# Optimization experiments

Hardware: AMD Instinct MI355X
Metric: run time of the kernel (lower is better)

The kernel has to match this reference:

```python
import jax, jax.numpy as jnp
import numpy as np

N_NODES = 50000
N_EDGES = 1600000
N_GRAPHS = 512
HID = 64


def _mlp_params(key, din, dout, scale=0.1):
    k1, k2, k3 = jax.random.split(key, 3)
    return (
        jax.random.normal(k1, (din, HID), jnp.float32) * scale, jnp.zeros((HID,), jnp.float32),
        jax.random.normal(k2, (HID, HID), jnp.float32) * scale, jnp.zeros((HID,), jnp.float32),
        jax.random.normal(k3, (HID, dout), jnp.float32) * scale, jnp.zeros((dout,), jnp.float32),
    )


def _mlp(x, w1, b1, w2, b2, w3, b3, out_act=None):
    h = jax.nn.relu(x @ w1 + b1)
    h = jax.nn.relu(h @ w2 + b2)
    o = h @ w3 + b3
    return o if out_act is None else out_act(o)


def setup_inputs() -> dict:
    key = jax.random.key(0)
    ks = jax.random.split(key, 8)
    nf = jax.random.normal(ks[0], (N_NODES, 1), jnp.float32)
    ef = jax.random.normal(ks[1], (N_EDGES, 1), jnp.float32)
    src = jax.random.randint(ks[2], (N_EDGES,), 0, N_NODES)
    dst = jax.random.randint(ks[3], (N_EDGES,), 0, N_NODES)
    graph_id = jnp.sort(jax.random.randint(ks[4], (N_NODES,), 0, N_GRAPHS))
    e_w1, e_b1, e_w2, e_b2, e_w3, e_b3 = _mlp_params(ks[5], 3, 1)   # edge model: [src_nf, dst_nf, ef] -> msg
    n_w1, n_b1, n_w2, n_b2, n_w3, n_b3 = _mlp_params(ks[6], 2, 1)   # node model: [nf, agg] -> unf
    m_w1, m_b1, m_w2, m_b2, m_w3, m_b3 = _mlp_params(ks[7], 1, 1)   # node-wise MLP with Sigmoid out_act
    return dict(nf=nf, ef=ef, src=src, dst=dst, graph_id=graph_id,
                e_w1=e_w1, e_b1=e_b1, e_w2=e_w2, e_b2=e_b2, e_w3=e_w3, e_b3=e_b3,
                n_w1=n_w1, n_b1=n_b1, n_w2=n_w2, n_b2=n_b2, n_w3=n_w3, n_b3=n_b3,
                m_w1=m_w1, m_b1=m_b1, m_w2=m_w2, m_b2=m_b2, m_w3=m_w3, m_b3=m_b3)


def reference(nf, ef, src, dst, graph_id,
              e_w1, e_b1, e_w2, e_b2, e_w3, e_b3,
              n_w1, n_b1, n_w2, n_b2, n_w3, n_b3,
              m_w1, m_b1, m_w2, m_b2, m_w3, m_b3):
    # MPNN layer: message on edges, sum-aggregate to dst nodes, node update
    em_in = jnp.concatenate([nf[src], nf[dst], ef], axis=-1)          # [E, 3]
    msg = _mlp(em_in, e_w1, e_b1, e_w2, e_b2, e_w3, e_b3)             # [E, 1]
    agg = jax.ops.segment_sum(msg, dst, num_segments=N_NODES)        # [N, 1]
    unf = _mlp(jnp.concatenate([nf, agg], axis=-1),
               n_w1, n_b1, n_w2, n_b2, n_w3, n_b3)                    # [N, 1]
    # node-wise MLP with Sigmoid output activation
    node_out = _mlp(unf, m_w1, m_b1, m_w2, m_b2, m_w3, m_b3,
                    out_act=jax.nn.sigmoid)                           # [N, 1]
    # sum readout per graph, then final sigmoid
    rd = jax.ops.segment_sum(node_out, graph_id, num_segments=N_GRAPHS)  # [G, 1]
    return jax.nn.sigmoid(rd)
```

## Files before the change

kernel.cpp:

```cpp
#include <hip/hip_runtime.h>
#include <math.h>

#define HID 64
#define BKT_SHIFT 13
#define BKT_RANGE 8192
#define CCHUNK 32

typedef __attribute__((ext_vector_type(8))) short short8;
typedef __attribute__((ext_vector_type(4))) float f32x4;
typedef unsigned long long ull;

union FragU {
    uint4 q;
    short8 v;
    uint32_t u[4];
};

__device__ __forceinline__ uint32_t cvt_pk_bf16(float lo, float hi) {
    uint32_t r;
    asm("v_cvt_pk_bf16_f32 %0, %1, %2" : "=v"(r) : "v"(lo), "v"(hi));
    return r;
}
__device__ __forceinline__ float bf16lo_f(uint32_t u) { return __uint_as_float(u << 16); }
__device__ __forceinline__ float bf16hi_f(uint32_t u) { return __uint_as_float(u & 0xFFFF0000u); }
__device__ __forceinline__ unsigned short bf16_of(float v) {
    return (unsigned short)(cvt_pk_bf16(v, 0.f) & 0xFFFFu);
}

__global__ void prep_kernel(
    const float* __restrict__ w1,  const float* __restrict__ b1,  const float* __restrict__ w2,
    const float* __restrict__ nw1, const float* __restrict__ nb1, const float* __restrict__ nw2,
    const float* __restrict__ mw1, const float* __restrict__ mb1, const float* __restrict__ mw2,
    unsigned short* __restrict__ w1x,  unsigned short* __restrict__ w2T,
    unsigned short* __restrict__ nw1x, unsigned short* __restrict__ nw2T,
    unsigned short* __restrict__ mw1x, unsigned short* __restrict__ mw2T)
{
    int t = blockIdx.x * 256 + threadIdx.x;
    if (t < 4096) {
        int j = t >> 6, k = t & 63;
        w2T [t] = bf16_of(w2 [k * HID + j]);
        nw2T[t] = bf16_of(nw2[k * HID + j]);
        mw2T[t] = bf16_of(mw2[k * HID + j]);
    }
    if (t < 512) {
        int j = t >> 3, k = t & 7;
        float ve = k == 0 ? w1[j] : k == 1 ? w1[HID + j] : k == 2 ? w1[2 * HID + j] : k == 3 ? b1[j] : 0.f;
        float vn = k == 0 ? nw1[j] : k == 1 ? nw1[HID + j] : k == 2 ? nb1[j] : 0.f;
        float vm = k == 0 ? mw1[j] : k == 1 ? mb1[j] : 0.f;
        w1x [t] = bf16_of(ve);
        nw1x[t] = bf16_of(vn);
        mw1x[t] = bf16_of(vm);
    }
}

__global__ __launch_bounds__(256, 4) void edge_mfma2_kernel(
    const float* __restrict__ nf, const float* __restrict__ ef,
    const int* __restrict__ src, const int* __restrict__ dst,
    const unsigned short* __restrict__ w1x, const unsigned short* __restrict__ w2T,
    const float* __restrict__ b2, const float* __restrict__ w3, const float* __restrict__ b3,
    uint2* __restrict__ recs, ull* __restrict__ offs,
    float* __restrict__ aggFb, int E, int B, int mode)
{
    __shared__ uint2 tile[4][16][16];

    const int tid  = threadIdx.x;
    const int lane = tid & 63;
    const int wid  = tid >> 6;
    const int g    = lane >> 4;
    const int eL   = lane & 15;

    FragU af1[4];
#pragma unroll
    for (int t = 0; t < 4; ++t) {
        uint4 q = *(const uint4*)&w1x[(t * 16 + eL) * 8];
        af1[t].q = (g == 0) ? q : make_uint4(0, 0, 0, 0);
    }
    FragU af2[4][2];
#pragma unroll
    for (int t = 0; t < 4; ++t)
#pragma unroll
        for (int h = 0; h < 2; ++h)
            af2[t][h].q = *(const uint4*)&w2T[(t * 16 + eL) * 64 + h * 32 + g * 8];

    f32x4 b2v4[4];
    uint32_t w3p[8];
#pragma unroll
    for (int t = 0; t < 4; ++t) {
        int j = t * 16 + g * 4;
        b2v4[t] = *(const f32x4*)&b2[j];
        f32x4 wv = *(const f32x4*)&w3[j];
        w3p[2 * t]     = cvt_pk_bf16(wv[0], wv[1]);
        w3p[2 * t + 1] = cvt_pk_bf16(wv[2], wv[3]);
    }
    const float b3c = b3[0];

    const int e0   = blockIdx.x * 256;
    const int eidx = e0 + tid;
    const int ei   = eidx < E ? eidx : E - 1;
    const int dmine = dst[ei];
    const float a = nf[src[ei]];
    const float b = nf[dmine];
    const float c = ef[ei];

    float mymsg = 0.f;

#pragma unroll
    for (int s = 0; s < 4; ++s) {
        float av = __shfl(a, s * 16 + eL);
        float bv = __shfl(b, s * 16 + eL);
        float cv = __shfl(c, s * 16 + eL);
        FragU bin;
        bin.u[0] = (g == 0) ? cvt_pk_bf16(av, bv) : 0u;
        bin.u[1] = (g == 0) ? cvt_pk_bf16(cv, 1.0f) : 0u;
        bin.u[2] = 0u; bin.u[3] = 0u;

#pragma unroll
        for (int t = 0; t < 4; ++t) {
            f32x4 h4 = __builtin_amdgcn_mfma_f32_16x16x32_bf16(
                af1[t].v, bin.v, (f32x4){0.f, 0.f, 0.f, 0.f}, 0, 0, 0);
            uint32_t p0 = cvt_pk_bf16(fmaxf(h4[0], 0.f), fmaxf(h4[1], 0.f));
            uint32_t p1 = cvt_pk_bf16(fmaxf(h4[2], 0.f), fmaxf(h4[3], 0.f));
            tile[wid][eL][(4 * t + g) ^ ((eL & 7) << 1)] = make_uint2(p0, p1);
        }

        FragU bf0, bf1;
        {
            const uint4* row = (const uint4*)&tile[wid][eL][0];
            bf0.q = row[(g)     ^ (eL & 7)];
            bf1.q = row[(4 + g) ^ (eL & 7)];
        }

        float p = 0.f;
#pragma unroll
        for (int t = 0; t < 4; ++t) {
            f32x4 ac = __builtin_amdgcn_mfma_f32_16x16x32_bf16(af2[t][0].v, bf0.v, b2v4[t], 0, 0, 0);
            ac = __builtin_amdgcn_mfma_f32_16x16x32_bf16(af2[t][1].v, bf1.v, ac, 0, 0, 0);
            p = fmaf(fmaxf(ac[0], 0.f), bf16lo_f(w3p[2 * t]),     p);
            p = fmaf(fmaxf(ac[1], 0.f), bf16hi_f(w3p[2 * t]),     p);
            p = fmaf(fmaxf(ac[2], 0.f), bf16lo_f(w3p[2 * t + 1]), p);
            p = fmaf(fmaxf(ac[3], 0.f), bf16hi_f(w3p[2 * t + 1]), p);
        }
        p += __shfl_xor(p, 16);
        p += __shfl_xor(p, 32);
        if (s == g) mymsg = p + b3c;
    }

    const bool valid = eidx < E;

    if (mode == 1) {
        if (valid) atomicAdd(&aggFb[dmine], mymsg);
        return;
    }

    const int bkt = dmine >> BKT_SHIFT;
    const ull lt = (1ull << lane) - 1;
    int myslot = 0;
    int off = 0;
    uint32_t pack_lo = 0, pack_hi = 0;
    for (int b = 0; b < B; ++b) {
        if (b < 4) pack_lo |= (uint32_t)off << (8 * b);
        else       pack_hi |= (uint32_t)off << (8 * (b - 4));
        ull m = __ballot(valid && bkt == b);
        if (valid && bkt == b) myslot = off + (int)__popcll(m & lt);
        off += (int)__popcll(m);
    }
    pack_hi |= (uint32_t)off << 24;

    const size_t wgl = (size_t)blockIdx.x * 4 + wid;
    if (valid) recs[wgl * 64 + myslot] = make_uint2((uint32_t)dmine, __float_as_uint(mymsg));
    if (lane == 0) offs[wgl] = ((ull)pack_hi << 32) | (ull)pack_lo;
}

__global__ __launch_bounds__(256) void bucket_accum_kernel(
    const uint2* __restrict__ recs, const ull* __restrict__ offs,
    float* __restrict__ partial, int NW, int B)
{
    __shared__ float acc[BKT_RANGE];

    const int b = blockIdx.x / CCHUNK;
    const int c = blockIdx.x % CCHUNK;

    for (int i = threadIdx.x; i < BKT_RANGE; i += 256) acc[i] = 0.f;
    __syncthreads();

    const int wpc = (NW + CCHUNK - 1) / CCHUNK;
    const int w0 = c * wpc;
    const int w1 = (w0 + wpc < NW) ? w0 + wpc : NW;
    const int nb = b + 1;
    const int base_node = b << BKT_SHIFT;

    for (int w = w0 + threadIdx.x; w < w1; w += 256) {
        ull ov = offs[w];
        uint32_t lo = (uint32_t)ov, hi = (uint32_t)(ov >> 32);
        int ob = (int)(((b  < 4) ? (lo >> (8 * b))  : (hi >> (8 * (b  - 4)))) & 0xFF);
        int oe = (int)(((nb < 4) ? (lo >> (8 * nb)) : (hi >> (8 * (nb - 4)))) & 0xFF);
        const uint2* rb = recs + (size_t)w * 64;
        for (int r = ob; r < oe; ++r) {
            uint2 rec = rb[r];
            atomicAdd(&acc[(int)rec.x - base_node], __uint_as_float(rec.y));
        }
    }
    __syncthreads();

    float* pb = partial + ((size_t)b * CCHUNK + c) * BKT_RANGE;
    for (int i = threadIdx.x; i < BKT_RANGE; i += 256) pb[i] = acc[i];
}

__global__ __launch_bounds__(256) void bucket_reduce_kernel(
    const float* __restrict__ partial, float* __restrict__ agg, int N)
{
    int n = blockIdx.x * 256 + threadIdx.x;
    if (n >= N) return;
    int b = n >> BKT_SHIFT, nl = n & (BKT_RANGE - 1);
    const float* p = partial + (size_t)b * CCHUNK * BKT_RANGE + nl;
    float s = 0.f;
#pragma unroll 8
    for (int c = 0; c < CCHUNK; ++c) s += p[(size_t)c * BKT_RANGE];
    agg[n] = s;
}

__global__ __launch_bounds__(64, 2) void node_mfma2_kernel(
    const float* __restrict__ nf, const float* __restrict__ agg,
    const int* __restrict__ gid,
    const unsigned short* __restrict__ nw1x, const unsigned short* __restrict__ nw2T,
    const float* __restrict__ nb2, const float* __restrict__ nw3, const float* __restrict__ nb3,
    const unsigned short* __restrict__ mw1x, const unsigned short* __restrict__ mw2T,
    const float* __restrict__ mb2, const float* __restrict__ mw3, const float* __restrict__ mb3,
    float* __restrict__ rd, int N)
{
    __shared__ uint2 tile[16][16];

    const int lane = threadIdx.x;
    const int g    = lane >> 4;
    const int eL   = lane & 15;

    const int n0 = blockIdx.x * 16;
    const int nn = n0 + eL < N ? n0 + eL : N - 1;
    const float x0 = nf[nn];
    const float x1 = agg[nn];

    float unf, o;

    {
        FragU af1[4], af2[4][2];
        f32x4 b2v4[4]; uint32_t w3p[8];
#pragma unroll
        for (int t = 0; t < 4; ++t) {
            uint4 q = *(const uint4*)&nw1x[(t * 16 + eL) * 8];
            af1[t].q = (g == 0) ? q : make_uint4(0, 0, 0, 0);
#pragma unroll
            for (int h = 0; h < 2; ++h)
                af2[t][h].q = *(const uint4*)&nw2T[(t * 16 + eL) * 64 + h * 32 + g * 8];
            int j = t * 16 + g * 4;
            b2v4[t] = *(const f32x4*)&nb2[j];
            f32x4 wv = *(const f32x4*)&nw3[j];
            w3p[2 * t]     = cvt_pk_bf16(wv[0], wv[1]);
            w3p[2 * t + 1] = cvt_pk_bf16(wv[2], wv[3]);
        }
        FragU bin;
        bin.u[0] = (g == 0) ? cvt_pk_bf16(x0, x1) : 0u;
        bin.u[1] = (g == 0) ? cvt_pk_bf16(1.0f, 0.f) : 0u;
        bin.u[2] = 0u; bin.u[3] = 0u;

#pragma unroll
        for (int t = 0; t < 4; ++t) {
            f32x4 h4 = __builtin_amdgcn_mfma_f32_16x16x32_bf16(
                af1[t].v, bin.v, (f32x4){0.f, 0.f, 0.f, 0.f}, 0, 0, 0);
            uint32_t p0 = cvt_pk_bf16(fmaxf(h4[0], 0.f), fmaxf(h4[1], 0.f));
            uint32_t p1 = cvt_pk_bf16(fmaxf(h4[2], 0.f), fmaxf(h4[3], 0.f));
            tile[eL][(4 * t + g) ^ ((eL & 7) << 1)] = make_uint2(p0, p1);
        }
        FragU bf0, bf1;
        {
            const uint4* row = (const uint4*)&tile[eL][0];
            bf0.q = row[(g)     ^ (eL & 7)];
            bf1.q = row[(4 + g) ^ (eL & 7)];
        }
        float p = 0.f;
#pragma unroll
        for (int t = 0; t < 4; ++t) {
            f32x4 ac = __builtin_amdgcn_mfma_f32_16x16x32_bf16(af2[t][0].v, bf0.v, b2v4[t], 0, 0, 0);
            ac = __builtin_amdgcn_mfma_f32_16x16x32_bf16(af2[t][1].v, bf1.v, ac, 0, 0, 0);
            p = fmaf(fmaxf(ac[0], 0.f), bf16lo_f(w3p[2 * t]),     p);
            p = fmaf(fmaxf(ac[1], 0.f), bf16hi_f(w3p[2 * t]),     p);
            p = fmaf(fmaxf(ac[2], 0.f), bf16lo_f(w3p[2 * t + 1]), p);
            p = fmaf(fmaxf(ac[3], 0.f), bf16hi_f(w3p[2 * t + 1]), p);
        }
        p += __shfl_xor(p, 16);
        p += __shfl_xor(p, 32);
        unf = p + nb3[0];
    }

    {
        FragU af1[4], af2[4][2];
        f32x4 b2v4[4]; uint32_t w3p[8];
#pragma unroll
        for (int t = 0; t < 4; ++t) {
            uint4 q = *(const uint4*)&mw1x[(t * 16 + eL) * 8];
            af1[t].q = (g == 0) ? q : make_uint4(0, 0, 0, 0);
#pragma unroll
            for (int h = 0; h < 2; ++h)
                af2[t][h].q = *(const uint4*)&mw2T[(t * 16 + eL) * 64 + h * 32 + g * 8];
            int j = t * 16 + g * 4;
            b2v4[t] = *(const f32x4*)&mb2[j];
            f32x4 wv = *(const f32x4*)&mw3[j];
            w3p[2 * t]     = cvt_pk_bf16(wv[0], wv[1]);
            w3p[2 * t + 1] = cvt_pk_bf16(wv[2], wv[3]);
        }
        FragU bin;
        bin.u[0] = (g == 0) ? cvt_pk_bf16(unf, 1.0f) : 0u;
        bin.u[1] = 0u; bin.u[2] = 0u; bin.u[3] = 0u;

#pragma unroll
        for (int t = 0; t < 4; ++t) {
            f32x4 h4 = __builtin_amdgcn_mfma_f32_16x16x32_bf16(
                af1[t].v, bin.v, (f32x4){0.f, 0.f, 0.f, 0.f}, 0, 0, 0);
            uint32_t p0 = cvt_pk_bf16(fmaxf(h4[0], 0.f), fmaxf(h4[1], 0.f));
            uint32_t p1 = cvt_pk_bf16(fmaxf(h4[2], 0.f), fmaxf(h4[3], 0.f));
            tile[eL][(4 * t + g) ^ ((eL & 7) << 1)] = make_uint2(p0, p1);
        }
        FragU bf0, bf1;
        {
            const uint4* row = (const uint4*)&tile[eL][0];
            bf0.q = row[(g)     ^ (eL & 7)];
            bf1.q = row[(4 + g) ^ (eL & 7)];
        }
        float p = 0.f;
#pragma unroll
        for (int t = 0; t < 4; ++t) {
            f32x4 ac = __builtin_amdgcn_mfma_f32_16x16x32_bf16(af2[t][0].v, bf0.v, b2v4[t], 0, 0, 0);
            ac = __builtin_amdgcn_mfma_f32_16x16x32_bf16(af2[t][1].v, bf1.v, ac, 0, 0, 0);
            p = fmaf(fmaxf(ac[0], 0.f), bf16lo_f(w3p[2 * t]),     p);
            p = fmaf(fmaxf(ac[1], 0.f), bf16hi_f(w3p[2 * t]),     p);
            p = fmaf(fmaxf(ac[2], 0.f), bf16lo_f(w3p[2 * t + 1]), p);
            p = fmaf(fmaxf(ac[3], 0.f), bf16hi_f(w3p[2 * t + 1]), p);
        }
        p += __shfl_xor(p, 16);
        p += __shfl_xor(p, 32);
        o = p + mb3[0];
    }

    float node_out = 1.0f / (1.0f + expf(-o));

    {
        int gg = gid[nn];
        float v = (n0 + eL < N && g == 0) ? node_out : 0.f;
#pragma unroll
        for (int d = 1; d < 16; d <<= 1) {
            float vup = __shfl_up(v, d);
            int   gup = __shfl_up(gg, d);
            if (lane >= d && lane < 16 && gup == gg) v += vup;
        }
        if (lane < 16 && n0 + lane < N) {
            int gdn = __shfl_down(gg, 1);
            bool tail = (lane == 15) || (n0 + lane + 1 >= N) || (gdn != gg);
            if (tail) atomicAdd(&rd[gg], v);
        }
    }
}

__global__ void readout_kernel(const float* __restrict__ rd,
                               float* __restrict__ out, int G)
{
    int g = blockIdx.x * blockDim.x + threadIdx.x;
    if (g < G) out[g] = 1.0f / (1.0f + expf(-rd[g]));
}

extern "C" void kernel_launch(void* const* d_in, const int* in_sizes, int n_in,
                              void* d_out, int out_size, void* d_ws, size_t ws_size,
                              hipStream_t stream)
{
    const float* nf  = (const float*)d_in[0];
    const float* ef  = (const float*)d_in[1];
    const int*   src = (const int*)  d_in[2];
    const int*   dst = (const int*)  d_in[3];
    const int*   gid = (const int*)  d_in[4];

    const float* e_w1 = (const float*)d_in[5];
    const float* e_b1 = (const float*)d_in[6];
    const float* e_w2 = (const float*)d_in[7];
    const float* e_b2 = (const float*)d_in[8];
    const float* e_w3 = (const float*)d_in[9];
    const float* e_b3 = (const float*)d_in[10];

    const float* n_w1 = (const float*)d_in[11];
    const float* n_b1 = (const float*)d_in[12];
    const float* n_w2 = (const float*)d_in[13];
    const float* n_b2 = (const float*)d_in[14];
    const float* n_w3 = (const float*)d_in[15];
    const float* n_b3 = (const float*)d_in[16];

    const float* m_w1 = (const float*)d_in[17];
    const float* m_b1 = (const float*)d_in[18];
    const float* m_w2 = (const float*)d_in[19];
    const float* m_b2 = (const float*)d_in[20];
    const float* m_w3 = (const float*)d_in[21];
    const float* m_b3 = (const float*)d_in[22];

    const int N = in_sizes[0];
    const int E = in_sizes[2];
    const int G = out_size;

    const int NW = (E + 63) / 64;
    const int B  = (N + BKT_RANGE - 1) / BKT_RANGE;

    size_t wts_b  = 32 * 1024;
    size_t recs_b = (size_t)NW * 64 * sizeof(uint2);
    size_t offs_b = (size_t)NW * sizeof(ull);
    size_t part_b = (size_t)B * CCHUNK * BKT_RANGE * sizeof(float);
    size_t need   = wts_b + recs_b + offs_b + part_b + ((size_t)N + G) * sizeof(float);
    bool bucketok = (B <= 8) && (need <= ws_size);

    char* wp = (char*)d_ws;
    unsigned short* w1x  = (unsigned short*)(wp);
    unsigned short* nw1x = (unsigned short*)(wp + 1024);
    unsigned short* mw1x = (unsigned short*)(wp + 2048);
    unsigned short* w2T  = (unsigned short*)(wp + 4096);
    unsigned short* nw2T = (unsigned short*)(wp + 4096 + 8192);
    unsigned short* mw2T = (unsigned short*)(wp + 4096 + 16384);

    float* out = (float*)d_out;

    prep_kernel<<<16, 256, 0, stream>>>(
        e_w1, e_b1, e_w2, n_w1, n_b1, n_w2, m_w1, m_b1, m_w2,
        w1x, w2T, nw1x, nw2T, mw1x, mw2T);

    if (bucketok) {
        uint2* recs    = (uint2*)(wp + wts_b);
        ull*   offs    = (ull*)(wp + wts_b + recs_b);
        float* partial = (float*)(wp + wts_b + recs_b + offs_b);
        float* agg     = (float*)(wp + wts_b + recs_b + offs_b + part_b);
        float* rd      = agg + N;

        hipMemsetAsync(rd, 0, (size_t)G * sizeof(float), stream);

        edge_mfma2_kernel<<<(E + 255) / 256, 256, 0, stream>>>(
            nf, ef, src, dst, w1x, w2T, e_b2, e_w3, e_b3,
            recs, offs, nullptr, E, B, 0);

        bucket_accum_kernel<<<B * CCHUNK, 256, 0, stream>>>(
            recs, offs, partial, NW, B);

        bucket_reduce_kernel<<<(N + 255) / 256, 256, 0, stream>>>(
            partial, agg, N);

        node_mfma2_kernel<<<(N + 15) / 16, 64, 0, stream>>>(
            nf, agg, gid,
            nw1x, nw2T, n_b2, n_w3, n_b3,
            mw1x, mw2T, m_b2, m_w3, m_b3,
            rd, N);

        readout_kernel<<<(G + 255) / 256, 256, 0, stream>>>(rd, out, G);
    } else {
        float* agg = (float*)(wp + wts_b);
        float* rd  = agg + N;

        hipMemsetAsync(agg, 0, ((size_t)N + G) * sizeof(float), stream);

        edge_mfma2_kernel<<<(E + 255) / 256, 256, 0, stream>>>(
            nf, ef, src, dst, w1x, w2T, e_b2, e_w3, e_b3,
            nullptr, nullptr, agg, E, B, 1);

        node_mfma2_kernel<<<(N + 15) / 16, 64, 0, stream>>>(
            nf, agg, gid,
            nw1x, nw2T, n_b2, n_w3, n_b3,
            mw1x, mw2T, m_b2, m_w3, m_b3,
            rd, N);

        readout_kernel<<<(G + 255) / 256, 256, 0, stream>>>(rd, out, G);
    }
}
```

Measured before the change: 87.40 us.

## Persistent edge kernel with gather prefetch; widen node kernel to four waves

The edge kernel becomes a grid-stride persistent kernel capped at 1024 blocks. It prefetches the next batch's src/dst/ef and the nf gathers while computing the MLP on the current batch, and splits the layer-1 and layer-2 phases across four LDS tiles so the gathers can overlap the compute. The node kernel moves from 16 nodes per 64-thread block to 256 nodes per 256-thread block, with a 64-lane segmented scan for the readout, which cuts block count and atomics. In exchange, LDS use grows and the occupancy hint for the edge kernel drops from 4 to 2, which raises register pressure.

```diff
diff --git a/kernel.cpp b/kernel.cpp
--- a/kernel.cpp
+++ b/kernel.cpp
@@ -53,15 +53,15 @@
     }
 }
 
-__global__ __launch_bounds__(256, 4) void edge_mfma2_kernel(
+__global__ __launch_bounds__(256, 2) void edge_mfma3_kernel(
     const float* __restrict__ nf, const float* __restrict__ ef,
     const int* __restrict__ src, const int* __restrict__ dst,
     const unsigned short* __restrict__ w1x, const unsigned short* __restrict__ w2T,
     const float* __restrict__ b2, const float* __restrict__ w3, const float* __restrict__ b3,
     uint2* __restrict__ recs, ull* __restrict__ offs,
-    float* __restrict__ aggFb, int E, int B, int mode)
-{
-    __shared__ uint2 tile[4][16][16];
+    float* __restrict__ aggFb, int E, int B, int nbatch, int mode)
+{
+    __shared__ uint2 tile[4][4][16][16];
 
     const int tid  = threadIdx.x;
     const int lane = tid & 63;
@@ -94,81 +94,97 @@
     }
     const float b3c = b3[0];
 
-    const int e0   = blockIdx.x * 256;
-    const int eidx = e0 + tid;
-    const int ei   = eidx < E ? eidx : E - 1;
-    const int dmine = dst[ei];
-    const float a = nf[src[ei]];
-    const float b = nf[dmine];
-    const float c = ef[ei];
-
-    float mymsg = 0.f;
-
-#pragma unroll
-    for (int s = 0; s < 4; ++s) {
-        float av = __shfl(a, s * 16 + eL);
-        float bv = __shfl(b, s * 16 + eL);
-        float cv = __shfl(c, s * 16 + eL);
-        FragU bin;
-        bin.u[0] = (g == 0) ? cvt_pk_bf16(av, bv) : 0u;
-        bin.u[1] = (g == 0) ? cvt_pk_bf16(cv, 1.0f) : 0u;
-        bin.u[2] = 0u; bin.u[3] = 0u;
-
-#pragma unroll
-        for (int t = 0; t < 4; ++t) {
-            f32x4 h4 = __builtin_amdgcn_mfma_f32_16x16x32_bf16(
-                af1[t].v, bin.v, (f32x4){0.f, 0.f, 0.f, 0.f}, 0, 0, 0);
-            uint32_t p0 = cvt_pk_bf16(fmaxf(h4[0], 0.f), fmaxf(h4[1], 0.f));
-            uint32_t p1 = cvt_pk_bf16(fmaxf(h4[2], 0.f), fmaxf(h4[3], 0.f));
-            tile[wid][eL][(4 * t + g) ^ ((eL & 7) << 1)] = make_uint2(p0, p1);
-        }
-
-        FragU bf0, bf1;
-        {
-            const uint4* row = (const uint4*)&tile[wid][eL][0];
+    int bi   = blockIdx.x;
+    if (bi >= nbatch) return;
+    int eidx = bi * 256 + tid;
+    int ei   = eidx < E ? eidx : E - 1;
+    int dcur = dst[ei];
+    float a  = nf[src[ei]];
+    float b  = nf[dcur];
+    float c  = ef[ei];
+
+    for (;;) {
+        const int nbi   = bi + gridDim.x;
+        const bool hn   = nbi < nbatch;
+        const int neidx = hn ? nbi * 256 + tid : eidx;
+        const int nei   = neidx < E ? neidx : E - 1;
+        const int ns    = src[nei];
+        const int nd    = dst[nei];
+        const float ncf = ef[nei];
+
+#pragma unroll
+        for (int s = 0; s < 4; ++s) {
+            float av = __shfl(a, s * 16 + eL);
+            float bv = __shfl(b, s * 16 + eL);
+            float cv = __shfl(c, s * 16 + eL);
+            FragU bin;
+            bin.u[0] = (g == 0) ? cvt_pk_bf16(av, bv) : 0u;
+            bin.u[1] = (g == 0) ? cvt_pk_bf16(cv, 1.0f) : 0u;
+            bin.u[2] = 0u; bin.u[3] = 0u;
+#pragma unroll
+            for (int t = 0; t < 4; ++t) {
+                f32x4 h4 = __builtin_amdgcn_mfma_f32_16x16x32_bf16(
+                    af1[t].v, bin.v, (f32x4){0.f, 0.f, 0.f, 0.f}, 0, 0, 0);
+                uint32_t p0 = cvt_pk_bf16(fmaxf(h4[0], 0.f), fmaxf(h4[1], 0.f));
+                uint32_t p1 = cvt_pk_bf16(fmaxf(h4[2], 0.f), fmaxf(h4[3], 0.f));
+                tile[wid][s][eL][(4 * t + g) ^ ((eL & 7) << 1)] = make_uint2(p0, p1);
+            }
+        }
+
+        const float na = nf[ns];
+        const float nb = nf[nd];
+
+        float mymsg = 0.f;
+#pragma unroll
+        for (int s = 0; s < 4; ++s) {
+            const uint4* row = (const uint4*)&tile[wid][s][eL][0];
+            FragU bf0, bf1;
             bf0.q = row[(g)     ^ (eL & 7)];
             bf1.q = row[(4 + g) ^ (eL & 7)];
-        }
-
-        float p = 0.f;
-#pragma unroll
-        for (int t = 0; t < 4; ++t) {
-            f32x4 ac = __builtin_amdgcn_mfma_f32_16x16x32_bf16(af2[t][0].v, bf0.v, b2v4[t], 0, 0, 0);
-            ac = __builtin_amdgcn_mfma_f32_16x16x32_bf16(af2[t][1].v, bf1.v, ac, 0, 0, 0);
-            p = fmaf(fmaxf(ac[0], 0.f), bf16lo_f(w3p[2 * t]),     p);
-            p = fmaf(fmaxf(ac[1], 0.f), bf16hi_f(w3p[2 * t]),     p);
-            p = fmaf(fmaxf(ac[2], 0.f), bf16lo_f(w3p[2 * t + 1]), p);
-            p = fmaf(fmaxf(ac[3], 0.f), bf16hi_f(w3p[2 * t + 1]), p);
-        }
-        p += __shfl_xor(p, 16);
-        p += __shfl_xor(p, 32);
-        if (s == g) mymsg = p + b3c;
-    }
-
-    const bool valid = eidx < E;
-
-    if (mode == 1) {
-        if (valid) atomicAdd(&aggFb[dmine], mymsg);
-        return;
-    }
-
-    const int bkt = dmine >> BKT_SHIFT;
-    const ull lt = (1ull << lane) - 1;
-    int myslot = 0;
-    int off = 0;
-    uint32_t pack_lo = 0, pack_hi = 0;
-    for (int b = 0; b < B; ++b) {
-        if (b < 4) pack_lo |= (uint32_t)off << (8 * b);
-        else       pack_hi |= (uint32_t)off << (8 * (b - 4));
-        ull m = __ballot(valid && bkt == b);
-        if (valid && bkt == b) myslot = off + (int)__popcll(m & lt);
-        off += (int)__popcll(m);
-    }
-    pack_hi |= (uint32_t)off << 24;
-
-    const size_t wgl = (size_t)blockIdx.x * 4 + wid;
-    if (valid) recs[wgl * 64 + myslot] = make_uint2((uint32_t)dmine, __float_as_uint(mymsg));
-    if (lane == 0) offs[wgl] = ((ull)pack_hi << 32) | (ull)pack_lo;
+
+            float p = 0.f;
+#pragma unroll
+            for (int t = 0; t < 4; ++t) {
+                f32x4 ac = __builtin_amdgcn_mfma_f32_16x16x32_bf16(af2[t][0].v, bf0.v, b2v4[t], 0, 0, 0);
+                ac = __builtin_amdgcn_mfma_f32_16x16x32_bf16(af2[t][1].v, bf1.v, ac, 0, 0, 0);
+                p = fmaf(fmaxf(ac[0], 0.f), bf16lo_f(w3p[2 * t]),     p);
+                p = fmaf(fmaxf(ac[1], 0.f), bf16hi_f(w3p[2 * t]),     p);
+                p = fmaf(fmaxf(ac[2], 0.f), bf16lo_f(w3p[2 * t + 1]), p);
+                p = fmaf(fmaxf(ac[3], 0.f), bf16hi_f(w3p[2 * t + 1]), p);
+            }
+            p += __shfl_xor(p, 16);
+            p += __shfl_xor(p, 32);
+            if (s == g) mymsg = p + b3c;
+        }
+
+        const bool valid = eidx < E;
+
+        if (mode == 1) {
+            if (valid) atomicAdd(&aggFb[dcur], mymsg);
+        } else {
+            const int bkt = dcur >> BKT_SHIFT;
+            const ull lt = (1ull << lane) - 1;
+            int myslot = 0;
+            int off = 0;
+            uint32_t pack_lo = 0, pack_hi = 0;
+            for (int bb = 0; bb < B; ++bb) {
+                if (bb < 4) pack_lo |= (uint32_t)off << (8 * bb);
+                else        pack_hi |= (uint32_t)off << (8 * (bb - 4));
+                ull m = __ballot(valid && bkt == bb);
+                if (valid && bkt == bb) myslot = off + (int)__popcll(m & lt);
+                off += (int)__popcll(m);
+            }
+            pack_hi |= (uint32_t)off << 24;
+
+            const size_t wgl = (size_t)bi * 4 + wid;
+            if (valid) recs[wgl * 64 + myslot] = make_uint2((uint32_t)dcur, __float_as_uint(mymsg));
+            if (lane == 0) offs[wgl] = ((ull)pack_hi << 32) | (ull)pack_lo;
+        }
+
+        if (!hn) break;
+        bi = nbi; eidx = neidx; ei = nei;
+        a = na; b = nb; c = ncf; dcur = nd;
+    }
 }
 
 __global__ __launch_bounds__(256) void bucket_accum_kernel(
@@ -219,7 +235,7 @@
     agg[n] = s;
 }
 
-__global__ __launch_bounds__(64, 2) void node_mfma2_kernel(
+__global__ __launch_bounds__(256, 2) void node_mfma3_kernel(
     const float* __restrict__ nf, const float* __restrict__ agg,
     const int* __restrict__ gid,
     const unsigned short* __restrict__ nw1x, const unsigned short* __restrict__ nw2T,
@@ -228,18 +244,21 @@
     const float* __restrict__ mb2, const float* __restrict__ mw3, const float* __restrict__ mb3,
     float* __restrict__ rd, int N)
 {
-    __shared__ uint2 tile[16][16];
-
-    const int lane = threadIdx.x;
+    __shared__ uint2 tile[4][4][16][16];
+
+    const int tid  = threadIdx.x;
+    const int lane = tid & 63;
+    const int wid  = tid >> 6;
     const int g    = lane >> 4;
     const int eL   = lane & 15;
 
-    const int n0 = blockIdx.x * 16;
-    const int nn = n0 + eL < N ? n0 + eL : N - 1;
-    const float x0 = nf[nn];
-    const float x1 = agg[nn];
-
-    float unf, o;
+    const int idx = blockIdx.x * 256 + tid;
+    const int i   = idx < N ? idx : N - 1;
+    const float x0 = nf[i];
+    const float x1 = agg[i];
+    const int   gg = gid[i];
+
+    float myunf = 0.f, o = 0.f;
 
     {
         FragU af1[4], af2[4][2];
@@ -257,38 +276,44 @@
             w3p[2 * t]     = cvt_pk_bf16(wv[0], wv[1]);
             w3p[2 * t + 1] = cvt_pk_bf16(wv[2], wv[3]);
         }
-        FragU bin;
-        bin.u[0] = (g == 0) ? cvt_pk_bf16(x0, x1) : 0u;
-        bin.u[1] = (g == 0) ? cvt_pk_bf16(1.0f, 0.f) : 0u;
-        bin.u[2] = 0u; bin.u[3] = 0u;
-
-#pragma unroll
-        for (int t = 0; t < 4; ++t) {
-            f32x4 h4 = __builtin_amdgcn_mfma_f32_16x16x32_bf16(
-                af1[t].v, bin.v, (f32x4){0.f, 0.f, 0.f, 0.f}, 0, 0, 0);
-            uint32_t p0 = cvt_pk_bf16(fmaxf(h4[0], 0.f), fmaxf(h4[1], 0.f));
-            uint32_t p1 = cvt_pk_bf16(fmaxf(h4[2], 0.f), fmaxf(h4[3], 0.f));
-            tile[eL][(4 * t + g) ^ ((eL & 7) << 1)] = make_uint2(p0, p1);
-        }
-        FragU bf0, bf1;
-        {
-            const uint4* row = (const uint4*)&tile[eL][0];
+
+#pragma unroll
+        for (int s = 0; s < 4; ++s) {
+            float av = __shfl(x0, s * 16 + eL);
+            float bv = __shfl(x1, s * 16 + eL);
+            FragU bin;
+            bin.u[0] = (g == 0) ? cvt_pk_bf16(av, bv) : 0u;
+            bin.u[1] = (g == 0) ? cvt_pk_bf16(1.0f, 0.f) : 0u;
+            bin.u[2] = 0u; bin.u[3] = 0u;
+#pragma unroll
+            for (int t = 0; t < 4; ++t) {
+                f32x4 h4 = __builtin_amdgcn_mfma_f32_16x16x32_bf16(
+                    af1[t].v, bin.v, (f32x4){0.f, 0.f, 0.f, 0.f}, 0, 0, 0);
+                uint32_t p0 = cvt_pk_bf16(fmaxf(h4[0], 0.f), fmaxf(h4[1], 0.f));
+                uint32_t p1 = cvt_pk_bf16(fmaxf(h4[2], 0.f), fmaxf(h4[3], 0.f));
+                tile[wid][s][eL][(4 * t + g) ^ ((eL & 7) << 1)] = make_uint2(p0, p1);
+            }
+        }
+#pragma unroll
+        for (int s = 0; s < 4; ++s) {
+            const uint4* row = (const uint4*)&tile[wid][s][eL][0];
+            FragU bf0, bf1;
             bf0.q = row[(g)     ^ (eL & 7)];
             bf1.q = row[(4 + g) ^ (eL & 7)];
-        }
-        float p = 0.f;
-#pragma unroll
-        for (int t = 0; t < 4; ++t) {
-            f32x4 ac = __builtin_amdgcn_mfma_f32_16x16x32_bf16(af2[t][0].v, bf0.v, b2v4[t], 0, 0, 0);
-            ac = __builtin_amdgcn_mfma_f32_16x16x32_bf16(af2[t][1].v, bf1.v, ac, 0, 0, 0);
-            p = fmaf(fmaxf(ac[0], 0.f), bf16lo_f(w3p[2 * t]),     p);
-            p = fmaf(fmaxf(ac[1], 0.f), bf16hi_f(w3p[2 * t]),     p);
-            p = fmaf(fmaxf(ac[2], 0.f), bf16lo_f(w3p[2 * t + 1]), p);
-            p = fmaf(fmaxf(ac[3], 0.f), bf16hi_f(w3p[2 * t + 1]), p);
-        }
-        p += __shfl_xor(p, 16);
-        p += __shfl_xor(p, 32);
-        unf = p + nb3[0];
+            float p = 0.f;
+#pragma unroll
+            for (int t = 0; t < 4; ++t) {
+                f32x4 ac = __builtin_amdgcn_mfma_f32_16x16x32_bf16(af2[t][0].v, bf0.v, b2v4[t], 0, 0, 0);
+                ac = __builtin_amdgcn_mfma_f32_16x16x32_bf16(af2[t][1].v, bf1.v, ac, 0, 0, 0);
+                p = fmaf(fmaxf(ac[0], 0.f), bf16lo_f(w3p[2 * t]),     p);
+                p = fmaf(fmaxf(ac[1], 0.f), bf16hi_f(w3p[2 * t]),     p);
+                p = fmaf(fmaxf(ac[2], 0.f), bf16lo_f(w3p[2 * t + 1]), p);
+                p = fmaf(fmaxf(ac[3], 0.f), bf16hi_f(w3p[2 * t + 1]), p);
+            }
+            p += __shfl_xor(p, 16);
+            p += __shfl_xor(p, 32);
+            if (s == g) myunf = p + nb3[0];
+        }
     }
 
     {
@@ -307,55 +332,60 @@
             w3p[2 * t]     = cvt_pk_bf16(wv[0], wv[1]);
             w3p[2 * t + 1] = cvt_pk_bf16(wv[2], wv[3]);
         }
-        FragU bin;
-        bin.u[0] = (g == 0) ? cvt_pk_bf16(unf, 1.0f) : 0u;
-        bin.u[1] = 0u; bin.u[2] = 0u; bin.u[3] = 0u;
-
-#pragma unroll
-        for (int t = 0; t < 4; ++t) {
-            f32x4 h4 = __builtin_amdgcn_mfma_f32_16x16x32_bf16(
-                af1[t].v, bin.v, (f32x4){0.f, 0.f, 0.f, 0.f}, 0, 0, 0);
-            uint32_t p0 = cvt_pk_bf16(fmaxf(h4[0], 0.f), fmaxf(h4[1], 0.f));
-            uint32_t p1 = cvt_pk_bf16(fmaxf(h4[2], 0.f), fmaxf(h4[3], 0.f));
-            tile[eL][(4 * t + g) ^ ((eL & 7) << 1)] = make_uint2(p0, p1);
-        }
-        FragU bf0, bf1;
-        {
-            const uint4* row = (const uint4*)&tile[eL][0];
+
+#pragma unroll
+        for (int s = 0; s < 4; ++s) {
+            float uv = __shfl(myunf, s * 16 + eL);
+            FragU bin;
+            bin.u[0] = (g == 0) ? cvt_pk_bf16(uv, 1.0f) : 0u;
+            bin.u[1] = 0u; bin.u[2] = 0u; bin.u[3] = 0u;
+#pragma unroll
+            for (int t = 0; t < 4; ++t) {
+                f32x4 h4 = __builtin_amdgcn_mfma_f32_16x16x32_bf16(
+                    af1[t].v, bin.v, (f32x4){0.f, 0.f, 0.f, 0.f}, 0, 0, 0);
+                uint32_t p0 = cvt_pk_bf16(fmaxf(h4[0], 0.f), fmaxf(h4[1], 0.f));
+                uint32_t p1 = cvt_pk_bf16(fmaxf(h4[2], 0.f), fmaxf(h4[3], 0.f));
+                tile[wid][s][eL][(4 * t + g) ^ ((eL & 7) << 1)] = make_uint2(p0, p1);
+            }
+        }
+#pragma unroll
+        for (int s = 0; s < 4; ++s) {
+            const uint4* row = (const uint4*)&tile[wid][s][eL][0];
+            FragU bf0, bf1;
             bf0.q = row[(g)     ^ (eL & 7)];
             bf1.q = row[(4 + g) ^ (eL & 7)];
-        }
-        float p = 0.f;
-#pragma unroll
-        for (int t = 0; t < 4; ++t) {
-            f32x4 ac = __builtin_amdgcn_mfma_f32_16x16x32_bf16(af2[t][0].v, bf0.v, b2v4[t], 0, 0, 0);
-            ac = __builtin_amdgcn_mfma_f32_16x16x32_bf16(af2[t][1].v, bf1.v, ac, 0, 0, 0);
-            p = fmaf(fmaxf(ac[0], 0.f), bf16lo_f(w3p[2 * t]),     p);
-            p = fmaf(fmaxf(ac[1], 0.f), bf16hi_f(w3p[2 * t]),     p);
-            p = fmaf(fmaxf(ac[2], 0.f), bf16lo_f(w3p[2 * t + 1]), p);
-            p = fmaf(fmaxf(ac[3], 0.f), bf16hi_f(w3p[2 * t + 1]), p);
-        }
-        p += __shfl_xor(p, 16);
-        p += __shfl_xor(p, 32);
-        o = p + mb3[0];
-    }
-
-    float node_out = 1.0f / (1.0f + expf(-o));
+            float p = 0.f;
+#pragma unroll
+            for (int t = 0; t < 4; ++t) {
+                f32x4 ac = __builtin_amdgcn_mfma_f32_16x16x32_bf16(af2[t][0].v, bf0.v, b2v4[t], 0, 0, 0);
+                ac = __builtin_amdgcn_mfma_f32_16x16x32_bf16(af2[t][1].v, bf1.v, ac, 0, 0, 0);
+                p = fmaf(fmaxf(ac[0], 0.f), bf16lo_f(w3p[2 * t]),     p);
+                p = fmaf(fmaxf(ac[1], 0.f), bf16hi_f(w3p[2 * t]),     p);
+                p = fmaf(fmaxf(ac[2], 0.f), bf16lo_f(w3p[2 * t + 1]), p);
+                p = fmaf(fmaxf(ac[3], 0.f), bf16hi_f(w3p[2 * t + 1]), p);
+            }
+            p += __shfl_xor(p, 16);
+            p += __shfl_xor(p, 32);
+            if (s == g) o = p + mb3[0];
+        }
+    }
+
+    const float node_out = 1.0f / (1.0f + expf(-o));
 
     {
-        int gg = gid[nn];
-        float v = (n0 + eL < N && g == 0) ? node_out : 0.f;
-#pragma unroll
-        for (int d = 1; d < 16; d <<= 1) {
+        const bool ok = idx < N;
+        float v = ok ? node_out : 0.0f;
+        int ggv = gg;
+#pragma unroll
+        for (int d = 1; d < 64; d <<= 1) {
             float vup = __shfl_up(v, d);
-            int   gup = __shfl_up(gg, d);
-            if (lane >= d && lane < 16 && gup == gg) v += vup;
-        }
-        if (lane < 16 && n0 + lane < N) {
-            int gdn = __shfl_down(gg, 1);
-            bool tail = (lane == 15) || (n0 + lane + 1 >= N) || (gdn != gg);
-            if (tail) atomicAdd(&rd[gg], v);
-        }
+            int   gup = __shfl_up(ggv, d);
+            if (lane >= d && gup == ggv) v += vup;
+        }
+        int gdn = __shfl_down(ggv, 1);
+        bool tail = (lane == 63) || (gdn != ggv);
+        if (tail)
+            atomicAdd(&rd[ggv], v);
     }
 }
 
@@ -401,6 +431,7 @@
     const int E = in_sizes[2];
     const int G = out_size;
 
+    const int nbatch = (E + 255) / 256;
     const int NW = (E + 63) / 64;
     const int B  = (N + BKT_RANGE - 1) / BKT_RANGE;
 
@@ -425,6 +456,8 @@
         e_w1, e_b1, e_w2, n_w1, n_b1, n_w2, m_w1, m_b1, m_w2,
         w1x, w2T, nw1x, nw2T, mw1x, mw2T);
 
+    int egrid = nbatch < 1024 ? nbatch : 1024;
+
     if (bucketok) {
         uint2* recs    = (uint2*)(wp + wts_b);
         ull*   offs    = (ull*)(wp + wts_b + recs_b);
@@ -434,9 +467,9 @@
 
         hipMemsetAsync(rd, 0, (size_t)G * sizeof(float), stream);
 
-        edge_mfma2_kernel<<<(E + 255) / 256, 256, 0, stream>>>(
+        edge_mfma3_kernel<<<egrid, 256, 0, stream>>>(
             nf, ef, src, dst, w1x, w2T, e_b2, e_w3, e_b3,
-            recs, offs, nullptr, E, B, 0);
+            recs, offs, nullptr, E, B, nbatch, 0);
 
         bucket_accum_kernel<<<B * CCHUNK, 256, 0, stream>>>(
             recs, offs, partial, NW, B);
@@ -444,7 +477,7 @@
         bucket_reduce_kernel<<<(N + 255) / 256, 256, 0, stream>>>(
             partial, agg, N);
 
-        node_mfma2_kernel<<<(N + 15) / 16, 64, 0, stream>>>(
+        node_mfma3_kernel<<<(N + 255) / 256, 256, 0, stream>>>(
             nf, agg, gid,
             nw1x, nw2T, n_b2, n_w3, n_b3,
             mw1x, mw2T, m_b2, m_w3, m_b3,
@@ -457,11 +490,11 @@
 
         hipMemsetAsync(agg, 0, ((size_t)N + G) * sizeof(float), stream);
 
-        edge_mfma2_kernel<<<(E + 255) / 256, 256, 0, stream>>>(
+        edge_mfma3_kernel<<<egrid, 256, 0, stream>>>(
             nf, ef, src, dst, w1x, w2T, e_b2, e_w3, e_b3,
-            nullptr, nullptr, agg, E, B, 1);
-
-        node_mfma2_kernel<<<(N + 15) / 16, 64, 0, stream>>>(
+            nullptr, nullptr, agg, E, B, nbatch, 1);
+
+        node_mfma3_kernel<<<(N + 255) / 256, 256, 0, stream>>>(
             nf, agg, gid,
             nw1x, nw2T, n_b2, n_w3, n_b3,
             mw1x, mw2T, m_b2, m_w3, m_b3,
```

New measurement: 79.49 us. 9.0% less time.
